# Optimization experiments

Hardware: AMD Instinct MI355X
Metric: run time of the kernel (lower is better)

## Reference

```python
import jax, jax.numpy as jnp
import numpy as np

B, H, W = 8, 64, 64
D_MODEL = 256
NUM_FREQS = 10
MLP_WIDTH = 256
N = 16384
IN_DIM = 2 + 4 * NUM_FREQS + 3 * D_MODEL  # enc(42) + 3 pyramid levels * d_model


def _dense_params(key, din, dout):
    kw, kb = jax.random.split(key)
    w = jax.random.normal(kw, (din, dout), jnp.float32) / np.sqrt(din)
    b = jnp.zeros((dout,), jnp.float32)
    return w, b


def setup_inputs() -> dict:
    key = jax.random.key(0)
    ks = jax.random.split(key, 8)
    feature_grid = jax.random.normal(ks[0], (B, H, W, D_MODEL), jnp.float32)
    coords = jax.random.uniform(ks[1], (N, 2), jnp.float32) * 2.0 - 1.0  # in [-1, 1]
    w0, b0 = _dense_params(ks[2], IN_DIM, MLP_WIDTH)
    w1, b1 = _dense_params(ks[3], MLP_WIDTH, MLP_WIDTH)
    w2, b2 = _dense_params(ks[4], MLP_WIDTH, MLP_WIDTH)
    w3, b3 = _dense_params(ks[5], MLP_WIDTH + IN_DIM, MLP_WIDTH)  # skip concat before mlp_3
    w_out, b_out = _dense_params(ks[6], MLP_WIDTH, 3)
    return {"feature_grid": feature_grid, "coords": coords,
            "w0": w0, "b0": b0, "w1": w1, "b1": b1, "w2": w2, "b2": b2,
            "w3": w3, "b3": b3, "w_out": w_out, "b_out": b_out}


def _posenc(x):
    # [x, sin(x*f0), cos(x*f0), sin(x*f1), cos(x*f1), ...] along last axis
    freqs = 2.0 ** jnp.arange(NUM_FREQS, dtype=jnp.float32) * jnp.pi
    parts = [x]
    for f in freqs:
        parts.append(jnp.sin(x * f))
        parts.append(jnp.cos(x * f))
    return jnp.concatenate(parts, axis=-1)


def _sample_pyramid(feature_grid, coords):
    Bv, Hv, Wv, C = feature_grid.shape
    pyramid = [feature_grid] + [
        jax.image.resize(feature_grid, (Bv, Hv // 2 ** i, Wv // 2 ** i, C), 'bilinear')
        for i in range(1, 3)
    ]
    sampled = []
    for level_grid in pyramid:
        level_shape = jnp.array(level_grid.shape[1:3], dtype=jnp.float32)
        cr = (coords + 1.0) / 2.0 * (level_shape - 1.0)  # [N, 2] -> pixel coords

        def sample_one_image(g_hwc):
            g_chw = g_hwc.transpose(2, 0, 1)  # [C, h, w]
            samp = jax.vmap(lambda g: jax.scipy.ndimage.map_coordinates(
                g, cr.T, order=1, mode='reflect'))(g_chw)  # [C, N]
            return samp.T  # [N, C]

        sampled.append(jax.vmap(sample_one_image)(level_grid))  # [B, N, C]
    return jnp.concatenate(sampled, axis=-1)  # [B, N, 3C]


def reference(feature_grid, coords, w0, b0, w1, b1, w2, b2, w3, b3, w_out, b_out):
    Bv = feature_grid.shape[0]
    enc = _posenc(coords)  # [N, 42]
    feats = _sample_pyramid(feature_grid, coords)  # [B, N, 3*d_model]
    enc_tiled = jnp.broadcast_to(enc[None], (Bv,) + enc.shape)
    x = jnp.concatenate([enc_tiled, feats], axis=-1)  # [B, N, IN_DIM]
    h = jax.nn.gelu(x @ w0 + b0)
    h = jax.nn.gelu(h @ w1 + b1)
    h = jax.nn.gelu(h @ w2 + b2)
    h = jnp.concatenate([h, x], axis=-1)  # skip connection at depth//2
    h = jax.nn.gelu(h @ w3 + b3)
    return jnp.tanh(h @ w_out + b_out)  # [B, N, 3]
```

## Files before the change

### kernel.cpp

```cpp
#include <hip/hip_runtime.h>
#include <math.h>

#define BFULL 8
#define HH 64
#define WWI 64
#define CC 256
#define NN 16384
#define INDIM 810
#define XP 832
#define K3P 1088
#define MLPW 256
#define FBM 128
#define HSTR 260
#define ASTR 40

typedef unsigned short u16;
typedef __attribute__((ext_vector_type(8))) short short8;
typedef __attribute__((ext_vector_type(4))) float f32x4;

__device__ __forceinline__ u16 f2bf(float f){
  union{float f; unsigned u;} v; v.f=f;
  unsigned r = v.u + 0x7FFFu + ((v.u>>16)&1u);
  return (u16)(r>>16);
}
__device__ __forceinline__ float bf2f(u16 h){
  union{unsigned u; float f;} v; v.u = ((unsigned)h)<<16; return v.f;
}
__device__ __forceinline__ float gelu_fast(float x){
  float z = 0.7978845608028654f*(x + 0.044715f*x*x*x);
  float e = __expf(2.0f*z);
  float t = 1.0f - 2.0f/(e + 1.0f);
  return 0.5f*x*(1.0f+t);
}

template<int OUTD, int RR>
__global__ __launch_bounds__(256) void resize_kernel(const float* __restrict__ in,
                                                     float* __restrict__ out){
  int bidx = blockIdx.x;
  int ox = bidx % OUTD;
  int oy = (bidx / OUTD) % OUTD;
  int b  = bidx / (OUTD*OUTD);
  int c = threadIdx.x;

  float sy = (oy + 0.5f)*RR - 0.5f;
  float sx = (ox + 0.5f)*RR - 0.5f;
  int jy0 = (int)floorf(sy) - RR + 1;
  int jx0 = (int)floorf(sx) - RR + 1;

  float wy[2*RR], wx[2*RR];
  int   jys[2*RR], jxs[2*RR];
  int cy=0, cx=0; float sumy=0.f, sumx=0.f;
  #pragma unroll
  for(int t=0;t<2*RR;t++){
    int j = jy0 + t;
    if(j>=0 && j<HH){
      float w = 1.0f - fabsf((float)j - sy)/(float)RR;
      if(w > 0.f){ jys[cy]=j; wy[cy]=w; sumy+=w; cy++; }
    }
  }
  #pragma unroll
  for(int t=0;t<2*RR;t++){
    int j = jx0 + t;
    if(j>=0 && j<WWI){
      float w = 1.0f - fabsf((float)j - sx)/(float)RR;
      if(w > 0.f){ jxs[cx]=j; wx[cx]=w; sumx+=w; cx++; }
    }
  }
  float acc = 0.f;
  for(int i=0;i<cy;i++)
    for(int j=0;j<cx;j++)
      acc += wy[i]*wx[j]*in[(((size_t)b*HH + jys[i])*WWI + jxs[j])*CC + c];
  acc /= (sumy*sumx);
  out[(((size_t)b*OUTD + oy)*OUTD + ox)*CC + c] = acc;
}

__global__ __launch_bounds__(256) void sample_encode_v2(
    const float* __restrict__ fg, const float* __restrict__ pyr1,
    const float* __restrict__ pyr2, const float* __restrict__ coords,
    u16* __restrict__ X, int m0, int mcount){
  int mi = blockIdx.x*2 + (threadIdx.x >> 7);
  if(mi >= mcount) return;
  int u = threadIdx.x & 127;
  int m = m0 + mi;
  int b = m / NN;
  int n = m % NN;
  float c0 = coords[(size_t)n*2 + 0];
  float c1 = coords[(size_t)n*2 + 1];
  u16* xrow = X + (size_t)mi*XP;

  if(u >= 64){
    if(u < 106){
      int p = u - 64;
      float v;
      if(p < 2){ v = (p==0) ? c0 : c1; }
      else {
        int k = (p-2) >> 2;
        int r = (p-2) & 3;
        float f = (float)(1u<<k) * 3.14159265358979323846f;
        float a = (r & 1) ? c1 : c0;
        v = (r < 2) ? sinf(a*f) : cosf(a*f);
      }
      xrow[p] = f2bf(v);
    } else {
      xrow[INDIM + (u - 106)] = 0;
    }
    return;
  }

  int c4 = u*4;
  const float* grids[3];
  grids[0] = fg   + (size_t)b*HH*WWI*CC;
  grids[1] = pyr1 + (size_t)b*32*32*CC;
  grids[2] = pyr2 + (size_t)b*16*16*CC;
  const int dims[3] = {64, 32, 16};

  #pragma unroll
  for(int lvl=0; lvl<3; lvl++){
    int d = dims[lvl];
    float yy = (c0 + 1.0f)*0.5f*(float)(d-1);
    float xx = (c1 + 1.0f)*0.5f*(float)(d-1);
    yy = fminf(fmaxf(yy, 0.0f), (float)(d-1));
    xx = fminf(fmaxf(xx, 0.0f), (float)(d-1));
    int y0 = (int)yy, x0 = (int)xx;
    int y1 = min(y0+1, d-1), x1 = min(x0+1, d-1);
    float ty = yy - (float)y0, tx = xx - (float)x0;
    const float* g = grids[lvl];
    float4 v00 = *(const float4*)&g[((size_t)y0*d + x0)*CC + c4];
    float4 v01 = *(const float4*)&g[((size_t)y0*d + x1)*CC + c4];
    float4 v10 = *(const float4*)&g[((size_t)y1*d + x0)*CC + c4];
    float4 v11 = *(const float4*)&g[((size_t)y1*d + x1)*CC + c4];
    float w00 = (1.f-ty)*(1.f-tx), w01 = (1.f-ty)*tx, w10 = ty*(1.f-tx), w11 = ty*tx;
    float r0 = w00*v00.x + w01*v01.x + w10*v10.x + w11*v11.x;
    float r1 = w00*v00.y + w01*v01.y + w10*v10.y + w11*v11.y;
    float r2 = w00*v00.z + w01*v01.z + w10*v10.z + w11*v11.z;
    float r3 = w00*v00.w + w01*v01.w + w10*v10.w + w11*v11.w;
    unsigned lo = (unsigned)f2bf(r0) | ((unsigned)f2bf(r1) << 16);
    unsigned hi = (unsigned)f2bf(r2) | ((unsigned)f2bf(r3) << 16);
    unsigned* dst = (unsigned*)&xrow[42 + lvl*CC + c4];
    dst[0] = lo; dst[1] = hi;
  }
}

__global__ __launch_bounds__(256) void wconv(const float* __restrict__ W,
                                             u16* __restrict__ Wb, int K, int Kp){
  int idx = blockIdx.x*256 + threadIdx.x;
  if(idx >= 256*Kp) return;
  int n = idx / Kp, k = idx % Kp;
  float v = (k < K) ? W[(size_t)k*MLPW + n] : 0.f;
  Wb[idx] = f2bf(v);
}

__global__ __launch_bounds__(256) void wconv_out(const float* __restrict__ wo,
                                                 u16* __restrict__ wob){
  int idx = blockIdx.x*256 + threadIdx.x;
  if(idx >= 16*256) return;
  int n = idx >> 8, k = idx & 255;
  float v = (n < 3) ? wo[(size_t)k*3 + n] : 0.f;
  wob[idx] = f2bf(v);
}

__global__ __launch_bounds__(512, 4) void fused_mlp(
    const u16* __restrict__ X,
    const u16* __restrict__ wb0, const u16* __restrict__ wb1,
    const u16* __restrict__ wb2, const u16* __restrict__ wb3,
    const u16* __restrict__ wob,
    const float* __restrict__ b0, const float* __restrict__ b1,
    const float* __restrict__ b2, const float* __restrict__ b3,
    const float* __restrict__ bo,
    float* __restrict__ out, int m0){
  __shared__ u16 Hs[FBM*HSTR];
  __shared__ u16 As[FBM*ASTR];

  int tid  = threadIdx.x;
  int lane = tid & 63, wv = tid >> 6;
  int wr = (wv>>2)*64, wc = (wv&3)*64;
  int rl = lane & 15;
  int koffe = (lane >> 4)*8;
  int rg = (lane >> 4)*4;

  size_t gm = (size_t)blockIdx.x*FBM;

  f32x4 acc[4][4];
  #pragma unroll
  for(int i=0;i<4;i++)
    #pragma unroll
    for(int j=0;j<4;j++) acc[i][j] = (f32x4){0.f,0.f,0.f,0.f};

  int srow = tid >> 2, skp = tid & 3;
  const u16* xbase = X + (gm + srow)*XP + skp*8;

  auto loadA = [&](const u16* aL, int astr, int ak, short8 af[4]){
    #pragma unroll
    for(int f=0; f<4; f++)
      af[f] = *(const short8*)&aL[(wr + f*16 + rl)*astr + ak + koffe];
  };
  auto loadB = [&](const u16* bw, int Kp2, int gk, short8 bf[4]){
    #pragma unroll
    for(int f=0; f<4; f++)
      bf[f] = *(const short8*)&bw[(size_t)(wc + f*16 + rl)*Kp2 + gk + koffe];
  };
  auto domfma = [&](short8 af[4], short8 bf[4]){
    #pragma unroll
    for(int i=0;i<4;i++)
      #pragma unroll
      for(int j=0;j<4;j++)
        acc[i][j] = __builtin_amdgcn_mfma_f32_16x16x32_bf16(af[i], bf[j], acc[i][j], 0,0,0);
  };
  auto epilogue = [&](const float* __restrict__ bias){
    __syncthreads();
    #pragma unroll
    for(int j=0;j<4;j++){
      int ncol = wc + j*16 + rl;
      float bv = bias[ncol];
      #pragma unroll
      for(int i=0;i<4;i++)
        #pragma unroll
        for(int r=0;r<4;r++){
          int row = wr + i*16 + rg + r;
          Hs[row*HSTR + ncol] = f2bf(gelu_fast(acc[i][j][r] + bv));
        }
    }
    __syncthreads();
    #pragma unroll
    for(int i=0;i<4;i++)
      #pragma unroll
      for(int j=0;j<4;j++) acc[i][j] = (f32x4){0.f,0.f,0.f,0.f};
  };
  auto xloop = [&](const u16* bw, int Kp2, int gbase){
    uint4 xv = *(const uint4*)(xbase);
    *(uint4*)&As[srow*ASTR + skp*8] = xv;
    __syncthreads();
    for(int kc=0; kc<26; kc++){
      uint4 xn;
      if(kc < 25) xn = *(const uint4*)(xbase + (kc+1)*32);
      short8 bf[4]; loadB(bw, Kp2, gbase + kc*32, bf);
      short8 af[4]; loadA(As, ASTR, 0, af);
      domfma(af, bf);
      __syncthreads();
      if(kc < 25) *(uint4*)&As[srow*ASTR + skp*8] = xn;
      __syncthreads();
    }
  };
  auto hloop = [&](const u16* bw, int Kp2, int gbase){
    #pragma unroll
    for(int kc=0; kc<8; kc++){
      short8 bf[4]; loadB(bw, Kp2, gbase + kc*32, bf);
      short8 af[4]; loadA(Hs, HSTR, kc*32, af);
      domfma(af, bf);
    }
  };

  xloop(wb0, XP, 0);
  epilogue(b0);
  hloop(wb1, 256, 0);
  epilogue(b1);
  hloop(wb2, 256, 0);
  epilogue(b2);
  hloop(wb3, K3P, 0);
  xloop(wb3, K3P, 256);
  epilogue(b3);

  if(wv < 2){
    f32x4 oa[4];
    #pragma unroll
    for(int i=0;i<4;i++) oa[i] = (f32x4){0.f,0.f,0.f,0.f};
    #pragma unroll
    for(int c=0;c<8;c++){
      short8 af[4];
      #pragma unroll
      for(int f=0; f<4; f++)
        af[f] = *(const short8*)&Hs[(wv*64 + f*16 + rl)*HSTR + c*32 + koffe];
      short8 bf1 = *(const short8*)&wob[(size_t)rl*256 + c*32 + koffe];
      #pragma unroll
      for(int i=0;i<4;i++)
        oa[i] = __builtin_amdgcn_mfma_f32_16x16x32_bf16(af[i], bf1, oa[i], 0,0,0);
    }
    if(rl < 3){
      float bv = bo[rl];
      #pragma unroll
      for(int i=0;i<4;i++)
        #pragma unroll
        for(int r=0;r<4;r++){
          size_t gr = (size_t)m0 + gm + wv*64 + i*16 + rg + r;
          out[gr*3 + rl] = tanhf(oa[i][r] + bv);
        }
    }
  }
}

extern "C" void kernel_launch(void* const* d_in, const int* in_sizes, int n_in,
                              void* d_out, int out_size, void* d_ws, size_t ws_size,
                              hipStream_t stream){
  const float* fg     = (const float*)d_in[0];
  const float* coords = (const float*)d_in[1];
  const float* w0 = (const float*)d_in[2];  const float* b0 = (const float*)d_in[3];
  const float* w1 = (const float*)d_in[4];  const float* b1 = (const float*)d_in[5];
  const float* w2 = (const float*)d_in[6];  const float* b2 = (const float*)d_in[7];
  const float* w3 = (const float*)d_in[8];  const float* b3 = (const float*)d_in[9];
  const float* wo = (const float*)d_in[10]; const float* bo = (const float*)d_in[11];
  float* out = (float*)d_out;

  char* ws = (char*)d_ws;
  size_t off = 0;
  auto alloc = [&](size_t bytes)->void*{
    void* p = ws + off;
    off += (bytes + 255) & ~(size_t)255;
    return p;
  };
  auto rnd = [](size_t bytes)->size_t{ return (bytes + 255) & ~(size_t)255; };

  size_t fixed =
      rnd((size_t)BFULL*32*32*CC*4) + rnd((size_t)BFULL*16*16*CC*4) +
      rnd((size_t)256*XP*2) + rnd((size_t)256*256*2) +
      rnd((size_t)256*256*2) + rnd((size_t)256*K3P*2) + rnd((size_t)16*256*2);

  const size_t Mtot = (size_t)BFULL*NN;
  size_t chunk = Mtot;
  while(chunk > 128){
    size_t need = fixed + rnd(chunk*(size_t)XP*2);
    if(need <= ws_size) break;
    chunk >>= 1;
  }
  size_t min_need = fixed + rnd(chunk*(size_t)XP*2);
  if(min_need > ws_size || (chunk % 128) != 0) return;

  float* pyr1 = (float*)alloc((size_t)BFULL*32*32*CC*4);
  float* pyr2 = (float*)alloc((size_t)BFULL*16*16*CC*4);
  u16* wb0 = (u16*)alloc((size_t)256*XP*2);
  u16* wb1 = (u16*)alloc((size_t)256*256*2);
  u16* wb2 = (u16*)alloc((size_t)256*256*2);
  u16* wb3 = (u16*)alloc((size_t)256*K3P*2);
  u16* wob = (u16*)alloc((size_t)16*256*2);
  u16* X  = (u16*)alloc(chunk*(size_t)XP*2);

  resize_kernel<32,2><<<dim3(BFULL*32*32), dim3(256), 0, stream>>>(fg, pyr1);
  resize_kernel<16,4><<<dim3(BFULL*16*16), dim3(256), 0, stream>>>(fg, pyr2);
  wconv<<<dim3((256*XP +255)/256), dim3(256), 0, stream>>>(w0, wb0, INDIM, XP);
  wconv<<<dim3((256*256 +255)/256), dim3(256), 0, stream>>>(w1, wb1, 256, 256);
  wconv<<<dim3((256*256 +255)/256), dim3(256), 0, stream>>>(w2, wb2, 256, 256);
  wconv<<<dim3((256*K3P +255)/256), dim3(256), 0, stream>>>(w3, wb3, MLPW+INDIM, K3P);
  wconv_out<<<dim3(16), dim3(256), 0, stream>>>(wo, wob);

  for(size_t m0=0; m0<Mtot; m0+=chunk){
    int mc = (int)chunk;
    sample_encode_v2<<<dim3(mc/2), dim3(256), 0, stream>>>(fg, pyr1, pyr2, coords, X, (int)m0, mc);
    fused_mlp<<<dim3(mc/FBM), dim3(512), 0, stream>>>(X, wb0, wb1, wb2, wb3, wob,
                                                      b0, b1, b2, b3, bo,
                                                      out, (int)m0);
  }
}
```

Measured before the change: 665.7 us.

## Load X operand fragments directly from global memory and stage output via LDS

The X-input GEMM phases (layer 0 and the skip half of layer 3) no longer stage tiles through a shared-memory buffer with two barriers per k-step. Each wave now reads its MFMA A fragments straight from global memory, so those barriers disappear at the cost of redundant global reads across the four waves that share rows. The final output is first written to a small LDS buffer and then stored by contiguous threads, so tanh and the global writes are coalesced.

```diff
diff --git a/kernel.cpp b/kernel.cpp
--- a/kernel.cpp
+++ b/kernel.cpp
@@ -12,7 +12,6 @@
 #define MLPW 256
 #define FBM 128
 #define HSTR 260
-#define ASTR 40
 
 typedef unsigned short u16;
 typedef __attribute__((ext_vector_type(8))) short short8;
@@ -169,7 +168,7 @@
     const float* __restrict__ bo,
     float* __restrict__ out, int m0){
   __shared__ u16 Hs[FBM*HSTR];
-  __shared__ u16 As[FBM*ASTR];
+  __shared__ float Os[FBM*4];
 
   int tid  = threadIdx.x;
   int lane = tid & 63, wv = tid >> 6;
@@ -186,14 +185,8 @@
     #pragma unroll
     for(int j=0;j<4;j++) acc[i][j] = (f32x4){0.f,0.f,0.f,0.f};
 
-  int srow = tid >> 2, skp = tid & 3;
-  const u16* xbase = X + (gm + srow)*XP + skp*8;
-
-  auto loadA = [&](const u16* aL, int astr, int ak, short8 af[4]){
-    #pragma unroll
-    for(int f=0; f<4; f++)
-      af[f] = *(const short8*)&aL[(wr + f*16 + rl)*astr + ak + koffe];
-  };
+  const u16* xA = X + (gm + wr + rl)*XP + koffe;
+
   auto loadB = [&](const u16* bw, int Kp2, int gk, short8 bf[4]){
     #pragma unroll
     for(int f=0; f<4; f++)
@@ -226,38 +219,57 @@
       #pragma unroll
       for(int j=0;j<4;j++) acc[i][j] = (f32x4){0.f,0.f,0.f,0.f};
   };
-  auto xloop = [&](const u16* bw, int Kp2, int gbase){
-    uint4 xv = *(const uint4*)(xbase);
-    *(uint4*)&As[srow*ASTR + skp*8] = xv;
-    __syncthreads();
-    for(int kc=0; kc<26; kc++){
-      uint4 xn;
-      if(kc < 25) xn = *(const uint4*)(xbase + (kc+1)*32);
-      short8 bf[4]; loadB(bw, Kp2, gbase + kc*32, bf);
-      short8 af[4]; loadA(As, ASTR, 0, af);
-      domfma(af, bf);
-      __syncthreads();
-      if(kc < 25) *(uint4*)&As[srow*ASTR + skp*8] = xn;
-      __syncthreads();
-    }
-  };
-  auto hloop = [&](const u16* bw, int Kp2, int gbase){
-    #pragma unroll
-    for(int kc=0; kc<8; kc++){
-      short8 bf[4]; loadB(bw, Kp2, gbase + kc*32, bf);
-      short8 af[4]; loadA(Hs, HSTR, kc*32, af);
-      domfma(af, bf);
-    }
-  };
-
-  xloop(wb0, XP, 0);
+
+  #pragma unroll 2
+  for(int kc=0; kc<26; kc++){
+    short8 af[4], bf[4];
+    #pragma unroll
+    for(int f=0; f<4; f++)
+      af[f] = *(const short8*)(xA + (size_t)(f*16)*XP + kc*32);
+    loadB(wb0, XP, kc*32, bf);
+    domfma(af, bf);
+  }
   epilogue(b0);
-  hloop(wb1, 256, 0);
+
+  #pragma unroll
+  for(int kc=0; kc<8; kc++){
+    short8 af[4], bf[4];
+    loadB(wb1, 256, kc*32, bf);
+    #pragma unroll
+    for(int f=0; f<4; f++)
+      af[f] = *(const short8*)&Hs[(wr + f*16 + rl)*HSTR + kc*32 + koffe];
+    domfma(af, bf);
+  }
   epilogue(b1);
-  hloop(wb2, 256, 0);
+  #pragma unroll
+  for(int kc=0; kc<8; kc++){
+    short8 af[4], bf[4];
+    loadB(wb2, 256, kc*32, bf);
+    #pragma unroll
+    for(int f=0; f<4; f++)
+      af[f] = *(const short8*)&Hs[(wr + f*16 + rl)*HSTR + kc*32 + koffe];
+    domfma(af, bf);
+  }
   epilogue(b2);
-  hloop(wb3, K3P, 0);
-  xloop(wb3, K3P, 256);
+
+  #pragma unroll
+  for(int kc=0; kc<8; kc++){
+    short8 af[4], bf[4];
+    loadB(wb3, K3P, kc*32, bf);
+    #pragma unroll
+    for(int f=0; f<4; f++)
+      af[f] = *(const short8*)&Hs[(wr + f*16 + rl)*HSTR + kc*32 + koffe];
+    domfma(af, bf);
+  }
+  #pragma unroll 2
+  for(int kc=0; kc<26; kc++){
+    short8 af[4], bf[4];
+    #pragma unroll
+    for(int f=0; f<4; f++)
+      af[f] = *(const short8*)(xA + (size_t)(f*16)*XP + kc*32);
+    loadB(wb3, K3P, 256 + kc*32, bf);
+    domfma(af, bf);
+  }
   epilogue(b3);
 
   if(wv < 2){
@@ -276,15 +288,17 @@
         oa[i] = __builtin_amdgcn_mfma_f32_16x16x32_bf16(af[i], bf1, oa[i], 0,0,0);
     }
     if(rl < 3){
-      float bv = bo[rl];
       #pragma unroll
       for(int i=0;i<4;i++)
         #pragma unroll
-        for(int r=0;r<4;r++){
-          size_t gr = (size_t)m0 + gm + wv*64 + i*16 + rg + r;
-          out[gr*3 + rl] = tanhf(oa[i][r] + bv);
-        }
-    }
+        for(int r=0;r<4;r++)
+          Os[(wv*64 + i*16 + rg + r)*4 + rl] = oa[i][r];
+    }
+  }
+  __syncthreads();
+  if(tid < FBM*3){
+    float v = Os[(tid/3)*4 + (tid%3)];
+    out[((size_t)m0 + gm)*3 + tid] = tanhf(v + bo[tid%3]);
   }
 }
 
```

New measurement: 786.6 us. +18.2%, slower.

## Double-buffer A and B tiles in LDS via direct global-to-LDS loads

Applied to the files above, without the earlier changes.

Weight (B) tiles, previously read directly from global memory into registers by every wave, are now staged into shared memory with global_load_lds, and so are the X tiles. Two buffers are used so the next k-chunk loads while the current one is consumed by MFMA. The output tanh store is routed through shared memory so global writes are coalesced. The larger LDS footprint lowers the occupancy hint from 4 to 2 blocks per CU, and the staged B tiles have an unpadded row stride that may cause bank conflicts.

```diff
diff --git a/kernel.cpp b/kernel.cpp
--- a/kernel.cpp
+++ b/kernel.cpp
@@ -12,7 +12,6 @@
 #define MLPW 256
 #define FBM 128
 #define HSTR 260
-#define ASTR 40
 
 typedef unsigned short u16;
 typedef __attribute__((ext_vector_type(8))) short short8;
@@ -31,6 +30,11 @@
   float e = __expf(2.0f*z);
   float t = 1.0f - 2.0f/(e + 1.0f);
   return 0.5f*x*(1.0f+t);
+}
+__device__ __forceinline__ void gl16(const u16* g, u16* l){
+  __builtin_amdgcn_global_load_lds(
+      (const __attribute__((address_space(1))) unsigned int*)g,
+      (__attribute__((address_space(3))) unsigned int*)l, 16, 0, 0);
 }
 
 template<int OUTD, int RR>
@@ -159,7 +163,7 @@
   wob[idx] = f2bf(v);
 }
 
-__global__ __launch_bounds__(512, 4) void fused_mlp(
+__global__ __launch_bounds__(512, 2) void fused_mlp(
     const u16* __restrict__ X,
     const u16* __restrict__ wb0, const u16* __restrict__ wb1,
     const u16* __restrict__ wb2, const u16* __restrict__ wb3,
@@ -168,8 +172,11 @@
     const float* __restrict__ b2, const float* __restrict__ b3,
     const float* __restrict__ bo,
     float* __restrict__ out, int m0){
-  __shared__ u16 Hs[FBM*HSTR];
-  __shared__ u16 As[FBM*ASTR];
+  __shared__ u16 pool[57856];
+  __shared__ float Os[FBM*4];
+  u16* Hs = pool;
+  u16* A0 = pool + 33280; u16* A1 = pool + 37376;
+  u16* B0 = pool + 41472; u16* B1 = pool + 49664;
 
   int tid  = threadIdx.x;
   int lane = tid & 63, wv = tid >> 6;
@@ -186,18 +193,28 @@
     #pragma unroll
     for(int j=0;j<4;j++) acc[i][j] = (f32x4){0.f,0.f,0.f,0.f};
 
-  int srow = tid >> 2, skp = tid & 3;
-  const u16* xbase = X + (gm + srow)*XP + skp*8;
-
-  auto loadA = [&](const u16* aL, int astr, int ak, short8 af[4]){
-    #pragma unroll
-    for(int f=0; f<4; f++)
-      af[f] = *(const short8*)&aL[(wr + f*16 + rl)*astr + ak + koffe];
-  };
-  auto loadB = [&](const u16* bw, int Kp2, int gk, short8 bf[4]){
-    #pragma unroll
-    for(int f=0; f<4; f++)
-      bf[f] = *(const short8*)&bw[(size_t)(wc + f*16 + rl)*Kp2 + gk + koffe];
+  int arow = tid >> 2, acol = (tid & 3)*8;
+  const u16* xsrc = X + (gm + arow)*XP + acol;
+  u16* wdst = pool + wv*512;
+
+  auto stageA = [&](u16* buf, int xk){
+    gl16(xsrc + xk, buf + wv*512);
+  };
+  auto stageB = [&](u16* buf, const u16* wb, int KpW, int gk){
+    gl16(wb + (size_t)arow*KpW + gk + acol,        buf + wv*512);
+    gl16(wb + (size_t)(128+arow)*KpW + gk + acol,  buf + 4096 + wv*512);
+  };
+  auto rdA = [&](const u16* buf, short8 af[4]){
+    #pragma unroll
+    for(int f=0;f<4;f++) af[f] = *(const short8*)&buf[(wr + f*16 + rl)*32 + koffe];
+  };
+  auto rdB = [&](const u16* buf, short8 bf[4]){
+    #pragma unroll
+    for(int f=0;f<4;f++) bf[f] = *(const short8*)&buf[(wc + f*16 + rl)*32 + koffe];
+  };
+  auto rdH = [&](int hk, short8 af[4]){
+    #pragma unroll
+    for(int f=0;f<4;f++) af[f] = *(const short8*)&Hs[(wr + f*16 + rl)*HSTR + hk + koffe];
   };
   auto domfma = [&](short8 af[4], short8 bf[4]){
     #pragma unroll
@@ -226,39 +243,39 @@
       #pragma unroll
       for(int j=0;j<4;j++) acc[i][j] = (f32x4){0.f,0.f,0.f,0.f};
   };
-  auto xloop = [&](const u16* bw, int Kp2, int gbase){
-    uint4 xv = *(const uint4*)(xbase);
-    *(uint4*)&As[srow*ASTR + skp*8] = xv;
+
+  auto xlayer = [&](const u16* wb, int KpW, int gbase){
+    stageA(A0, 0); stageB(B0, wb, KpW, gbase);
     __syncthreads();
-    for(int kc=0; kc<26; kc++){
-      uint4 xn;
-      if(kc < 25) xn = *(const uint4*)(xbase + (kc+1)*32);
-      short8 bf[4]; loadB(bw, Kp2, gbase + kc*32, bf);
-      short8 af[4]; loadA(As, ASTR, 0, af);
-      domfma(af, bf);
+    #pragma unroll 1
+    for(int kc=0; kc<26; kc+=2){
+      stageA(A1, (kc+1)*32); stageB(B1, wb, KpW, gbase+(kc+1)*32);
+      { short8 af[4], bf[4]; rdA(A0,af); rdB(B0,bf); domfma(af,bf); }
       __syncthreads();
-      if(kc < 25) *(uint4*)&As[srow*ASTR + skp*8] = xn;
+      if(kc+2 < 26){ stageA(A0, (kc+2)*32); stageB(B0, wb, KpW, gbase+(kc+2)*32); }
+      { short8 af[4], bf[4]; rdA(A1,af); rdB(B1,bf); domfma(af,bf); }
       __syncthreads();
     }
   };
-  auto hloop = [&](const u16* bw, int Kp2, int gbase){
-    #pragma unroll
-    for(int kc=0; kc<8; kc++){
-      short8 bf[4]; loadB(bw, Kp2, gbase + kc*32, bf);
-      short8 af[4]; loadA(Hs, HSTR, kc*32, af);
-      domfma(af, bf);
-    }
-  };
-
-  xloop(wb0, XP, 0);
-  epilogue(b0);
-  hloop(wb1, 256, 0);
-  epilogue(b1);
-  hloop(wb2, 256, 0);
-  epilogue(b2);
-  hloop(wb3, K3P, 0);
-  xloop(wb3, K3P, 256);
-  epilogue(b3);
+  auto hlayer = [&](const u16* wb, int KpW, int gbase){
+    stageB(B0, wb, KpW, gbase);
+    __syncthreads();
+    #pragma unroll 1
+    for(int kc=0; kc<8; kc+=2){
+      stageB(B1, wb, KpW, gbase+(kc+1)*32);
+      { short8 af[4], bf[4]; rdH(kc*32, af); rdB(B0,bf); domfma(af,bf); }
+      __syncthreads();
+      if(kc+2 < 8) stageB(B0, wb, KpW, gbase+(kc+2)*32);
+      { short8 af[4], bf[4]; rdH((kc+1)*32, af); rdB(B1,bf); domfma(af,bf); }
+      __syncthreads();
+    }
+  };
+
+  xlayer(wb0, XP, 0);          epilogue(b0);
+  hlayer(wb1, 256, 0);         epilogue(b1);
+  hlayer(wb2, 256, 0);         epilogue(b2);
+  hlayer(wb3, K3P, 0);
+  xlayer(wb3, K3P, 256);       epilogue(b3);
 
   if(wv < 2){
     f32x4 oa[4];
@@ -276,15 +293,17 @@
         oa[i] = __builtin_amdgcn_mfma_f32_16x16x32_bf16(af[i], bf1, oa[i], 0,0,0);
     }
     if(rl < 3){
-      float bv = bo[rl];
       #pragma unroll
       for(int i=0;i<4;i++)
         #pragma unroll
-        for(int r=0;r<4;r++){
-          size_t gr = (size_t)m0 + gm + wv*64 + i*16 + rg + r;
-          out[gr*3 + rl] = tanhf(oa[i][r] + bv);
-        }
-    }
+        for(int r=0;r<4;r++)
+          Os[(wv*64 + i*16 + rg + r)*4 + rl] = oa[i][r];
+    }
+  }
+  __syncthreads();
+  if(tid < FBM*3){
+    float v = Os[(tid/3)*4 + (tid%3)];
+    out[((size_t)m0 + gm)*3 + tid] = tanhf(v + bo[tid%3]);
   }
 }
 
```

Result: slower. 689.0 us (+3.5%).
